# Optimization experiments

Measured on AMD Instinct MI355X. Metric: run time of the kernel, lower is better.

The kernel has to match this reference:

```python
import jax, jax.numpy as jnp
import numpy as np

H = W = 256          # input_img_height (square images)
N_NODES = 8          # camera graph nodes
N_EDGES = 64         # ~fully connected directed graph
FEAT = 1024          # edge_feat_dim
BN_EPS = 1e-5


def setup_inputs() -> dict:
    key = jax.random.key(0)
    ks = jax.random.split(key, 8)
    d = {}
    d["x"] = jax.random.normal(ks[0], (N_NODES, 3 * H * W), dtype=jnp.float32)
    d["edge_index"] = jax.random.randint(ks[1], (2, N_EDGES), 0, N_NODES)
    # ResNet stem params (conv1 replaced to take 6 channels)
    d["conv1_w"] = jax.random.normal(ks[2], (64, 6, 7, 7), dtype=jnp.float32) * 0.05
    d["bn_gamma"] = jnp.ones((64,), jnp.float32)
    d["bn_beta"] = jnp.zeros((64,), jnp.float32)
    d["bn_mean"] = jnp.zeros((64,), jnp.float32)
    d["bn_var"] = jnp.ones((64,), jnp.float32)
    d["fc_w"] = jax.random.normal(ks[3], (FEAT, 64), dtype=jnp.float32) * 0.05
    d["fc_b"] = jnp.zeros((FEAT,), jnp.float32)
    d["fc_xyz_w"] = jax.random.normal(ks[4], (3, FEAT), dtype=jnp.float32) * 0.05
    d["fc_xyz_b"] = jnp.zeros((3,), jnp.float32)
    d["fc_wpqr_w"] = jax.random.normal(ks[5], (3, FEAT), dtype=jnp.float32) * 0.05
    d["fc_wpqr_b"] = jnp.zeros((3,), jnp.float32)
    return d


def _edge_extractor(ef, conv1_w, bn_gamma, bn_beta, bn_mean, bn_var, fc_w, fc_b):
    # conv1: 6->64, 7x7, stride 2, pad 3, no bias
    y = jax.lax.conv_general_dilated(
        ef, conv1_w, window_strides=(2, 2), padding=[(3, 3), (3, 3)],
        dimension_numbers=("NCHW", "OIHW", "NCHW"))
    # BatchNorm (inference form with running stats), fused scale/shift
    scale = (bn_gamma * jax.lax.rsqrt(bn_var + BN_EPS))[None, :, None, None]
    shift = (bn_beta - bn_mean * bn_gamma * jax.lax.rsqrt(bn_var + BN_EPS))[None, :, None, None]
    y = jax.nn.relu(y * scale + shift)
    # maxpool 3x3 stride 2 pad 1
    y = jax.lax.reduce_window(y, -jnp.inf, jax.lax.max,
                              (1, 1, 3, 3), (1, 1, 2, 2),
                              [(0, 0), (0, 0), (1, 1), (1, 1)])
    # AdaptiveAvgPool2d(1) + fc to edge_feat_dim
    y = jnp.mean(y, axis=(2, 3))                     # [E, 64]
    return y @ fc_w.T + fc_b                         # [E, FEAT]


def reference(x, edge_index, conv1_w, bn_gamma, bn_beta, bn_mean, bn_var,
              fc_w, fc_b, fc_xyz_w, fc_xyz_b, fc_wpqr_w, fc_wpqr_b):
    imgs = x.reshape(N_NODES, 3, H, W)
    # compute_edge_features, vectorized: gather min/max node per edge, concat channels
    nmin = jnp.min(edge_index, axis=0)               # [E]
    nmax = jnp.max(edge_index, axis=0)               # [E]
    edge_feat = jnp.concatenate([imgs[nmin], imgs[nmax]], axis=1)  # [E, 6, H, W]
    ef = _edge_extractor(edge_feat, conv1_w, bn_gamma, bn_beta, bn_mean, bn_var, fc_w, fc_b)
    ef = jax.nn.relu(ef)
    # droprate == 0 -> no dropout
    xyz = ef @ fc_xyz_w.T + fc_xyz_b                 # [E, 3]
    wpqr = ef @ fc_wpqr_w.T + fc_wpqr_b              # [E, 3]
    full = jnp.concatenate([xyz, wpqr], axis=1)      # [E, 6]
    return (full[:N_NODES], full)
```

## Files before the change

kernel.cpp:

```cpp
#include <hip/hip_runtime.h>
#include <hip/hip_bf16.h>

#define N_NODES 8
#define N_EDGES 64
#define CO 64
#define OH 128
#define OW 128
#define FEAT 1024
#define BN_EPS 1e-5f

#define OFF_POOLED 0
#define OFF_WB     16384
#define OFF_SHIFT  65536
#define OFF_A      65792
#define OFF_B      (65792 + 16777216)

typedef short bf16x8 __attribute__((ext_vector_type(8)));
typedef float f32x4  __attribute__((ext_vector_type(4)));

__device__ __forceinline__ unsigned short f2bf(float f) {
    unsigned u = __float_as_uint(f);
    u += 0x7fffu + ((u >> 16) & 1u);
    return (unsigned short)(u >> 16);
}
__device__ __forceinline__ float blo(unsigned u) { return __uint_as_float(u << 16); }
__device__ __forceinline__ float bhi(unsigned u) { return __uint_as_float(u & 0xffff0000u); }

__global__ __launch_bounds__(256) void repack_kernel(
        const float* __restrict__ w,
        const float* __restrict__ gamma, const float* __restrict__ beta,
        const float* __restrict__ mean,  const float* __restrict__ var,
        unsigned short* __restrict__ wb2, float* __restrict__ shiftb,
        float* __restrict__ pooled) {
    int idx = blockIdx.x * 256 + threadIdx.x;
    if (idx < 2 * 64 * 192) {
        int t = idx % 192;
        int c = (idx / 192) & 63;
        int h = idx / (192 * 64);
        int rr = t >> 3, kx = t & 7;
        float val = 0.f;
        if (rr < 21 && kx < 7) {
            int ci = rr / 7, ky = rr % 7;
            float sc = gamma[c] * rsqrtf(var[c] + BN_EPS);
            val = w[((c * 6 + h * 3 + ci) * 7 + ky) * 7 + kx] * sc;
        }
        wb2[(rr * 128 + h * 64 + c) * 8 + kx] = f2bf(val);
    }
    if (idx < 64) {
        float sc = gamma[idx] * rsqrtf(var[idx] + BN_EPS);
        shiftb[idx] = beta[idx] - mean[idx] * sc;
    }
    if (idx < 64 * 64) pooled[idx] = 0.f;
}

#define RS_W 136

__global__ __launch_bounds__(512, 4) void conv_kernel(
        const float* __restrict__ x, const unsigned short* __restrict__ wb2,
        const float* __restrict__ shiftb,
        unsigned short* __restrict__ A2, unsigned short* __restrict__ B2) {
    int n  = blockIdx.x >> 7;
    int oy = blockIdx.x & 127;
    int t  = threadIdx.x;

    __shared__ __align__(16) char smem[34816];
    unsigned* rawu = (unsigned*)smem;

    const float* img = x + (size_t)n * (3 * 256 * 256);
    for (int k = t; k < 24 * RS_W; k += 512) {
        int u  = k % RS_W;
        int rr = k / RS_W;
        unsigned val = 0u;
        if (rr < 21 && u < 131) {
            int ci = (rr * 147) >> 10;
            int ky = rr - ci * 7;
            int iy = 2 * oy - 3 + ky;
            if ((unsigned)iy < 256u) {
                int c0 = 2 * u - 3;
                const float* row = img + (ci * 256 + iy) * 256;
                float f0 = ((unsigned)c0 < 256u) ? row[c0] : 0.f;
                float f1 = ((unsigned)(c0 + 1) < 256u) ? row[c0 + 1] : 0.f;
                val = (unsigned)f2bf(f0) | ((unsigned)f2bf(f1) << 16);
            }
        }
        rawu[k] = val;
    }
    __syncthreads();

    int wv = t >> 6, lane = t & 63;
    int h  = wv & 1, wg = wv >> 1;
    int quad = lane >> 4, m = lane & 15;

    f32x4 acc[4][2];
#pragma unroll
    for (int ct = 0; ct < 4; ++ct) {
        acc[ct][0] = (f32x4){0.f, 0.f, 0.f, 0.f};
        acc[ct][1] = (f32x4){0.f, 0.f, 0.f, 0.f};
    }

    const bf16x8* wbv = (const bf16x8*)wb2;

#pragma unroll 2
    for (int s = 0; s < 6; ++s) {
        int rq = 4 * s + quad;
        bf16x8 afrag[2];
#pragma unroll
        for (int nt = 0; nt < 2; ++nt) {
            int ox = 32 * wg + 16 * nt + m;
            int base = rq * RS_W + ox;
            union { unsigned u[4]; bf16x8 v; } bb;
            bb.u[0] = rawu[base];     bb.u[1] = rawu[base + 1];
            bb.u[2] = rawu[base + 2]; bb.u[3] = rawu[base + 3];
            afrag[nt] = bb.v;
        }
#pragma unroll
        for (int ct = 0; ct < 4; ++ct) {
            bf16x8 wfrag = wbv[rq * 128 + h * 64 + 16 * ct + m];
#pragma unroll
            for (int nt = 0; nt < 2; ++nt)
                acc[ct][nt] = __builtin_amdgcn_mfma_f32_16x16x32_bf16(
                                  afrag[nt], wfrag, acc[ct][nt], 0, 0, 0);
        }
    }

    float sh[4] = {0.f, 0.f, 0.f, 0.f};
    if (h) {
#pragma unroll
        for (int ct = 0; ct < 4; ++ct) sh[ct] = shiftb[16 * ct + m];
    }

    __syncthreads();
    unsigned short* T = (unsigned short*)smem;

#pragma unroll
    for (int ct = 0; ct < 4; ++ct) {
        int chp = h * 64 + 16 * ct + m;
#pragma unroll
        for (int nt = 0; nt < 2; ++nt) {
            int px0 = 32 * wg + 16 * nt + 4 * quad;
            float v0 = acc[ct][nt][0] + sh[ct];
            float v1 = acc[ct][nt][1] + sh[ct];
            float v2 = acc[ct][nt][2] + sh[ct];
            float v3 = acc[ct][nt][3] + sh[ct];
            uint2 pk;
            pk.x = (unsigned)f2bf(v0) | ((unsigned)f2bf(v1) << 16);
            pk.y = (unsigned)f2bf(v2) | ((unsigned)f2bf(v3) << 16);
            *(uint2*)&T[chp * 136 + px0] = pk;
        }
    }
    __syncthreads();

    int row = t >> 2, slot = t & 3;
    int hh = row >> 6, ch = row & 63;
    unsigned short* dst = (hh ? B2 : A2)
                        + ((size_t)(n * CO + ch) << 14) + (oy << 7) + slot * 32;
#pragma unroll
    for (int i = 0; i < 4; ++i)
        *(uint4*)(dst + i * 8) = *(uint4*)&T[row * 136 + slot * 32 + i * 8];
}

__global__ __launch_bounds__(256, 4) void pool_kernel(
        const unsigned short* __restrict__ A2,
        const unsigned short* __restrict__ B2,
        float* __restrict__ pooled) {
    int b  = blockIdx.x;
    int c  = b >> 4;
    int rt = b & 15;
    int t  = threadIdx.x;

    __shared__ unsigned short S[2 * 8 * 9 * 128];

    for (int k = t; k < 2304; k += 256) {
        int slot = k & 15;
        int r    = (k >> 4) % 9;
        int tn   = (k >> 4) / 9;
        int grow = 8 * rt - 1 + r;
        uint4 v = make_uint4(0u, 0u, 0u, 0u);
        if (grow >= 0) {
            const unsigned short* src = (tn >= 8) ? B2 : A2;
            int node = tn & 7;
            v = *(const uint4*)(src + ((size_t)(node * CO + c) << 14)
                                    + (grow << 7) + slot * 8);
        }
        *(uint4*)&S[tn * 1152 + (r << 7) + slot * 8] = v;
    }
    __syncthreads();

    int wv = t >> 6, lane = t & 63;
    int esub = lane >> 4, tc = lane & 15;

    for (int i = 0; i < 3; ++i) {
        int sidx = 12 * wv + 4 * i + esub;
        bool valid = sidx < 36;
        int ss = valid ? sidx : 0;
        int pi = 0, rem = ss;
        while (rem >= 8 - pi) { rem -= 8 - pi; ++pi; }
        int pj = pi + rem;
        const unsigned short* pa = &S[pi * 1152];
        const unsigned short* pb = &S[(8 + pj) * 1152];

        float mx[4][4];
#pragma unroll
        for (int p = 0; p < 4; ++p)
#pragma unroll
            for (int q = 0; q < 4; ++q) mx[p][q] = 0.f;

#pragma unroll
        for (int r = 0; r < 9; ++r) {
            uint4 ga = *(const uint4*)(pa + (r << 7) + tc * 8);
            uint4 gb = *(const uint4*)(pb + (r << 7) + tc * 8);
            float ha = 0.f, hb = 0.f;
            if (tc > 0) {
                ha = bhi(*(const unsigned*)(pa + (r << 7) + tc * 8 - 2));
                hb = bhi(*(const unsigned*)(pb + (r << 7) + tc * 8 - 2));
            }
            float z0 = ha + hb;
            float z1 = blo(ga.x) + blo(gb.x), z2 = bhi(ga.x) + bhi(gb.x);
            float z3 = blo(ga.y) + blo(gb.y), z4 = bhi(ga.y) + bhi(gb.y);
            float z5 = blo(ga.z) + blo(gb.z), z6 = bhi(ga.z) + bhi(gb.z);
            float z7 = blo(ga.w) + blo(gb.w), z8 = bhi(ga.w) + bhi(gb.w);
            float h0 = fmaxf(fmaxf(z0, z1), z2);
            float h1 = fmaxf(fmaxf(z2, z3), z4);
            float h2 = fmaxf(fmaxf(z4, z5), z6);
            float h3 = fmaxf(fmaxf(z6, z7), z8);
            if (r & 1) {
                int p = (r - 1) >> 1;
                mx[p][0] = fmaxf(mx[p][0], h0); mx[p][1] = fmaxf(mx[p][1], h1);
                mx[p][2] = fmaxf(mx[p][2], h2); mx[p][3] = fmaxf(mx[p][3], h3);
            } else {
                if (r >= 2) {
                    int p = (r >> 1) - 1;
                    mx[p][0] = fmaxf(mx[p][0], h0); mx[p][1] = fmaxf(mx[p][1], h1);
                    mx[p][2] = fmaxf(mx[p][2], h2); mx[p][3] = fmaxf(mx[p][3], h3);
                }
                if (r <= 6) {
                    int p = r >> 1;
                    mx[p][0] = fmaxf(mx[p][0], h0); mx[p][1] = fmaxf(mx[p][1], h1);
                    mx[p][2] = fmaxf(mx[p][2], h2); mx[p][3] = fmaxf(mx[p][3], h3);
                }
            }
        }

        float sum = 0.f;
#pragma unroll
        for (int p = 0; p < 4; ++p)
#pragma unroll
            for (int q = 0; q < 4; ++q) sum += fmaxf(mx[p][q], 0.f);

        sum += __shfl_down(sum, 8, 64);
        sum += __shfl_down(sum, 4, 64);
        sum += __shfl_down(sum, 2, 64);
        sum += __shfl_down(sum, 1, 64);
        if (tc == 0 && valid)
            atomicAdd(&pooled[((pi << 3) + pj) * 64 + c], sum);
    }
}

__global__ __launch_bounds__(256) void head_kernel(
        const int* __restrict__ ei, const float* __restrict__ pooled,
        const float* __restrict__ fc_w,   const float* __restrict__ fc_b,
        const float* __restrict__ xyz_w,  const float* __restrict__ xyz_b,
        const float* __restrict__ wpqr_w, const float* __restrict__ wpqr_b,
        float* __restrict__ out) {
    int e = blockIdx.x;
    int t = threadIdx.x;
    int a0 = ei[e], a1 = ei[N_EDGES + e];
    int code = (min(a0, a1) << 3) + max(a0, a1);
    __shared__ float pl[CO];
    if (t < CO) pl[t] = pooled[(code << 6) + t] * (1.f / 4096.f);
    __syncthreads();

    float s[6] = {0.f, 0.f, 0.f, 0.f, 0.f, 0.f};
#pragma unroll
    for (int ff = 0; ff < 4; ++ff) {
        int f = ff * 256 + t;
        const float* wr = fc_w + f * CO;
        float d = fc_b[f];
#pragma unroll
        for (int c = 0; c < CO; ++c) d = fmaf(pl[c], wr[c], d);
        d = fmaxf(d, 0.f);
#pragma unroll
        for (int r = 0; r < 3; ++r) {
            s[r]     = fmaf(d, xyz_w[r * FEAT + f],  s[r]);
            s[3 + r] = fmaf(d, wpqr_w[r * FEAT + f], s[3 + r]);
        }
    }
#pragma unroll
    for (int r = 0; r < 6; ++r)
#pragma unroll
        for (int off = 32; off > 0; off >>= 1)
            s[r] += __shfl_down(s[r], off, 64);

    __shared__ float red[4][6];
    if ((t & 63) == 0) {
#pragma unroll
        for (int r = 0; r < 6; ++r) red[t >> 6][r] = s[r];
    }
    __syncthreads();
    if (t < 6) {
        float v = red[0][t] + red[1][t] + red[2][t] + red[3][t];
        v += (t < 3) ? xyz_b[t] : wpqr_b[t - 3];
        out[48 + e * 6 + t] = v;
        if (e < 8) out[e * 6 + t] = v;
    }
}

extern "C" void kernel_launch(void* const* d_in, const int* in_sizes, int n_in,
                              void* d_out, int out_size, void* d_ws, size_t ws_size,
                              hipStream_t stream) {
    const float* x        = (const float*)d_in[0];
    const int*   ei       = (const int*)d_in[1];
    const float* conv1_w  = (const float*)d_in[2];
    const float* bn_gamma = (const float*)d_in[3];
    const float* bn_beta  = (const float*)d_in[4];
    const float* bn_mean  = (const float*)d_in[5];
    const float* bn_var   = (const float*)d_in[6];
    const float* fc_w     = (const float*)d_in[7];
    const float* fc_b     = (const float*)d_in[8];
    const float* xyz_w    = (const float*)d_in[9];
    const float* xyz_b    = (const float*)d_in[10];
    const float* wpqr_w   = (const float*)d_in[11];
    const float* wpqr_b   = (const float*)d_in[12];
    float* out = (float*)d_out;

    char* ws = (char*)d_ws;
    float*          pooled = (float*)(ws + OFF_POOLED);
    unsigned short* wb2    = (unsigned short*)(ws + OFF_WB);
    float*          shiftb = (float*)(ws + OFF_SHIFT);
    unsigned short* A2     = (unsigned short*)(ws + OFF_A);
    unsigned short* B2     = (unsigned short*)(ws + OFF_B);

    repack_kernel<<<96, 256, 0, stream>>>(conv1_w, bn_gamma, bn_beta, bn_mean,
                                          bn_var, wb2, shiftb, pooled);
    conv_kernel<<<1024, 512, 0, stream>>>(x, wb2, shiftb, A2, B2);
    pool_kernel<<<1024, 256, 0, stream>>>(A2, B2, pooled);
    head_kernel<<<64, 256, 0, stream>>>(ei, pooled, fc_w, fc_b,
                                        xyz_w, xyz_b, wpqr_w, wpqr_b, out);
}
```

Before: 137.8 us.

## Fuse four kernels into one persistent cooperative kernel with grid syncs

Replaces the repack, conv, pool and head launches with a single cooperative kernel of 256 blocks. Each block loops over four passes of conv rows and pool tiles, and grid.sync separates the stages. This is meant to remove launch overhead and the gaps between kernels. In exchange the grid is smaller, so each stage gets less parallelism and no overlap across passes, and the grid-wide barriers add their own cost.

```diff
diff --git a/kernel.cpp b/kernel.cpp
--- a/kernel.cpp
+++ b/kernel.cpp
@@ -1,5 +1,8 @@
 #include <hip/hip_runtime.h>
 #include <hip/hip_bf16.h>
+#include <hip/hip_cooperative_groups.h>
+
+namespace cg = cooperative_groups;
 
 #define N_NODES 8
 #define N_EDGES 64
@@ -15,6 +18,8 @@
 #define OFF_A      65792
 #define OFF_B      (65792 + 16777216)
 
+#define RS_W 136
+
 typedef short bf16x8 __attribute__((ext_vector_type(8)));
 typedef float f32x4  __attribute__((ext_vector_type(4)));
 
@@ -26,282 +31,294 @@
 __device__ __forceinline__ float blo(unsigned u) { return __uint_as_float(u << 16); }
 __device__ __forceinline__ float bhi(unsigned u) { return __uint_as_float(u & 0xffff0000u); }
 
-__global__ __launch_bounds__(256) void repack_kernel(
+__global__ __launch_bounds__(512, 4) void fused_kernel(
+        const float* __restrict__ x, const int* __restrict__ ei,
         const float* __restrict__ w,
         const float* __restrict__ gamma, const float* __restrict__ beta,
         const float* __restrict__ mean,  const float* __restrict__ var,
-        unsigned short* __restrict__ wb2, float* __restrict__ shiftb,
-        float* __restrict__ pooled) {
-    int idx = blockIdx.x * 256 + threadIdx.x;
-    if (idx < 2 * 64 * 192) {
-        int t = idx % 192;
-        int c = (idx / 192) & 63;
-        int h = idx / (192 * 64);
-        int rr = t >> 3, kx = t & 7;
-        float val = 0.f;
-        if (rr < 21 && kx < 7) {
-            int ci = rr / 7, ky = rr % 7;
-            float sc = gamma[c] * rsqrtf(var[c] + BN_EPS);
-            val = w[((c * 6 + h * 3 + ci) * 7 + ky) * 7 + kx] * sc;
-        }
-        wb2[(rr * 128 + h * 64 + c) * 8 + kx] = f2bf(val);
+        const float* __restrict__ fc_w,  const float* __restrict__ fc_b,
+        const float* __restrict__ xyz_w, const float* __restrict__ xyz_b,
+        const float* __restrict__ wpqr_w,const float* __restrict__ wpqr_b,
+        float* __restrict__ out,
+        float* __restrict__ pooled, unsigned short* __restrict__ wb2,
+        float* __restrict__ shiftb,
+        unsigned short* __restrict__ A2, unsigned short* __restrict__ B2) {
+    cg::grid_group grid = cg::this_grid();
+    int t   = threadIdx.x;
+    int blk = blockIdx.x;
+
+    __shared__ __align__(16) char smem[36864];
+
+    {
+        int idx = blk * 512 + t;
+        if (idx < 2 * 64 * 192) {
+            int tp = idx % 192;
+            int c  = (idx / 192) & 63;
+            int h  = idx / (192 * 64);
+            int rr = tp >> 3, kx = tp & 7;
+            float val = 0.f;
+            if (rr < 21 && kx < 7) {
+                int ci = rr / 7, ky = rr % 7;
+                float sc = gamma[c] * rsqrtf(var[c] + BN_EPS);
+                val = w[((c * 6 + h * 3 + ci) * 7 + ky) * 7 + kx] * sc;
+            }
+            wb2[(rr * 128 + h * 64 + c) * 8 + kx] = f2bf(val);
+        }
+        if (idx < 64) {
+            float sc = gamma[idx] * rsqrtf(var[idx] + BN_EPS);
+            shiftb[idx] = beta[idx] - mean[idx] * sc;
+        }
+        if (idx < 64 * 64) pooled[idx] = 0.f;
     }
-    if (idx < 64) {
-        float sc = gamma[idx] * rsqrtf(var[idx] + BN_EPS);
-        shiftb[idx] = beta[idx] - mean[idx] * sc;
+    __threadfence();
+    grid.sync();
+
+    {
+        unsigned* rawu = (unsigned*)smem;
+        int wv = t >> 6, lane = t & 63;
+        int h  = wv & 1, wg = wv >> 1;
+        int quad = lane >> 4, m = lane & 15;
+
+        for (int pass = 0; pass < 4; ++pass) {
+            int cb = pass * 256 + blk;
+            int n  = cb >> 7, oy = cb & 127;
+
+            const float* img = x + (size_t)n * (3 * 256 * 256);
+            for (int k = t; k < 24 * RS_W; k += 512) {
+                int u  = k % RS_W;
+                int rr = k / RS_W;
+                unsigned val = 0u;
+                if (rr < 21 && u < 131) {
+                    int ci = (rr * 147) >> 10;
+                    int ky = rr - ci * 7;
+                    int iy = 2 * oy - 3 + ky;
+                    if ((unsigned)iy < 256u) {
+                        int c0 = 2 * u - 3;
+                        const float* row = img + (ci * 256 + iy) * 256;
+                        float f0 = ((unsigned)c0 < 256u) ? row[c0] : 0.f;
+                        float f1 = ((unsigned)(c0 + 1) < 256u) ? row[c0 + 1] : 0.f;
+                        val = (unsigned)f2bf(f0) | ((unsigned)f2bf(f1) << 16);
+                    }
+                }
+                rawu[k] = val;
+            }
+            __syncthreads();
+
+            f32x4 acc[4][2];
+#pragma unroll
+            for (int ct = 0; ct < 4; ++ct) {
+                acc[ct][0] = (f32x4){0.f, 0.f, 0.f, 0.f};
+                acc[ct][1] = (f32x4){0.f, 0.f, 0.f, 0.f};
+            }
+
+            const bf16x8* wbv = (const bf16x8*)wb2;
+
+#pragma unroll 2
+            for (int s = 0; s < 6; ++s) {
+                int rq = 4 * s + quad;
+                bf16x8 afrag[2];
+#pragma unroll
+                for (int nt = 0; nt < 2; ++nt) {
+                    int ox = 32 * wg + 16 * nt + m;
+                    int base = rq * RS_W + ox;
+                    union { unsigned u[4]; bf16x8 v; } bb;
+                    bb.u[0] = rawu[base];     bb.u[1] = rawu[base + 1];
+                    bb.u[2] = rawu[base + 2]; bb.u[3] = rawu[base + 3];
+                    afrag[nt] = bb.v;
+                }
+#pragma unroll
+                for (int ct = 0; ct < 4; ++ct) {
+                    bf16x8 wfrag = wbv[rq * 128 + h * 64 + 16 * ct + m];
+#pragma unroll
+                    for (int nt = 0; nt < 2; ++nt)
+                        acc[ct][nt] = __builtin_amdgcn_mfma_f32_16x16x32_bf16(
+                                          afrag[nt], wfrag, acc[ct][nt], 0, 0, 0);
+                }
+            }
+
+            float sh[4] = {0.f, 0.f, 0.f, 0.f};
+            if (h) {
+#pragma unroll
+                for (int ct = 0; ct < 4; ++ct) sh[ct] = shiftb[16 * ct + m];
+            }
+
+            __syncthreads();
+            unsigned short* T = (unsigned short*)smem;
+
+#pragma unroll
+            for (int ct = 0; ct < 4; ++ct) {
+                int chp = h * 64 + 16 * ct + m;
+#pragma unroll
+                for (int nt = 0; nt < 2; ++nt) {
+                    int px0 = 32 * wg + 16 * nt + 4 * quad;
+                    float v0 = acc[ct][nt][0] + sh[ct];
+                    float v1 = acc[ct][nt][1] + sh[ct];
+                    float v2 = acc[ct][nt][2] + sh[ct];
+                    float v3 = acc[ct][nt][3] + sh[ct];
+                    uint2 pk;
+                    pk.x = (unsigned)f2bf(v0) | ((unsigned)f2bf(v1) << 16);
+                    pk.y = (unsigned)f2bf(v2) | ((unsigned)f2bf(v3) << 16);
+                    *(uint2*)&T[chp * 136 + px0] = pk;
+                }
+            }
+            __syncthreads();
+
+            int row = t >> 2, slot = t & 3;
+            int hh = row >> 6, ch = row & 63;
+            unsigned short* dst = (hh ? B2 : A2)
+                                + ((size_t)(n * CO + ch) << 14) + (oy << 7)
+                                + slot * 32;
+#pragma unroll
+            for (int i = 0; i < 4; ++i)
+                *(uint4*)(dst + i * 8) = *(uint4*)&T[row * 136 + slot * 32 + i * 8];
+            __syncthreads();
+        }
     }
-    if (idx < 64 * 64) pooled[idx] = 0.f;
-}
-
-#define RS_W 136
-
-__global__ __launch_bounds__(512, 4) void conv_kernel(
-        const float* __restrict__ x, const unsigned short* __restrict__ wb2,
-        const float* __restrict__ shiftb,
-        unsigned short* __restrict__ A2, unsigned short* __restrict__ B2) {
-    int n  = blockIdx.x >> 7;
-    int oy = blockIdx.x & 127;
-    int t  = threadIdx.x;
-
-    __shared__ __align__(16) char smem[34816];
-    unsigned* rawu = (unsigned*)smem;
-
-    const float* img = x + (size_t)n * (3 * 256 * 256);
-    for (int k = t; k < 24 * RS_W; k += 512) {
-        int u  = k % RS_W;
-        int rr = k / RS_W;
-        unsigned val = 0u;
-        if (rr < 21 && u < 131) {
-            int ci = (rr * 147) >> 10;
-            int ky = rr - ci * 7;
-            int iy = 2 * oy - 3 + ky;
-            if ((unsigned)iy < 256u) {
-                int c0 = 2 * u - 3;
-                const float* row = img + (ci * 256 + iy) * 256;
-                float f0 = ((unsigned)c0 < 256u) ? row[c0] : 0.f;
-                float f1 = ((unsigned)(c0 + 1) < 256u) ? row[c0 + 1] : 0.f;
-                val = (unsigned)f2bf(f0) | ((unsigned)f2bf(f1) << 16);
-            }
-        }
-        rawu[k] = val;
+    __threadfence();
+    grid.sync();
+
+    {
+        unsigned short* S = (unsigned short*)smem;
+        int wv = t >> 6, lane = t & 63;
+        int esub = lane >> 4, tc = lane & 15;
+
+        for (int pass = 0; pass < 4; ++pass) {
+            int pb = pass * 256 + blk;
+            int c  = pb >> 4;
+            int rt = pb & 15;
+
+            __syncthreads();
+            for (int k = t; k < 2304; k += 512) {
+                int slot = k & 15;
+                int r    = (k >> 4) % 9;
+                int tn   = (k >> 4) / 9;
+                int grow = 8 * rt - 1 + r;
+                uint4 v = make_uint4(0u, 0u, 0u, 0u);
+                if (grow >= 0) {
+                    const unsigned short* src = (tn >= 8) ? B2 : A2;
+                    int node = tn & 7;
+                    v = *(const uint4*)(src + ((size_t)(node * CO + c) << 14)
+                                            + (grow << 7) + slot * 8);
+                }
+                *(uint4*)&S[tn * 1152 + (r << 7) + slot * 8] = v;
+            }
+            __syncthreads();
+
+            for (int i = 0; i < 2; ++i) {
+                int slot0 = 32 * i + wv * 4;
+                if (slot0 >= 36) continue;
+                int sidx = slot0 + esub;
+                bool valid = sidx < 36;
+                int ss = valid ? sidx : 0;
+                int pi = 0, rem = ss;
+                while (rem >= 8 - pi) { rem -= 8 - pi; ++pi; }
+                int pj = pi + rem;
+                const unsigned short* pa  = &S[pi * 1152];
+                const unsigned short* pb2 = &S[(8 + pj) * 1152];
+
+                float mx[4][4];
+#pragma unroll
+                for (int p = 0; p < 4; ++p)
+#pragma unroll
+                    for (int q = 0; q < 4; ++q) mx[p][q] = 0.f;
+
+#pragma unroll
+                for (int r = 0; r < 9; ++r) {
+                    uint4 ga = *(const uint4*)(pa + (r << 7) + tc * 8);
+                    uint4 gb = *(const uint4*)(pb2 + (r << 7) + tc * 8);
+                    float ha = 0.f, hb = 0.f;
+                    if (tc > 0) {
+                        ha = bhi(*(const unsigned*)(pa + (r << 7) + tc * 8 - 2));
+                        hb = bhi(*(const unsigned*)(pb2 + (r << 7) + tc * 8 - 2));
+                    }
+                    float z0 = ha + hb;
+                    float z1 = blo(ga.x) + blo(gb.x), z2 = bhi(ga.x) + bhi(gb.x);
+                    float z3 = blo(ga.y) + blo(gb.y), z4 = bhi(ga.y) + bhi(gb.y);
+                    float z5 = blo(ga.z) + blo(gb.z), z6 = bhi(ga.z) + bhi(gb.z);
+                    float z7 = blo(ga.w) + blo(gb.w), z8 = bhi(ga.w) + bhi(gb.w);
+                    float h0 = fmaxf(fmaxf(z0, z1), z2);
+                    float h1 = fmaxf(fmaxf(z2, z3), z4);
+                    float h2 = fmaxf(fmaxf(z4, z5), z6);
+                    float h3 = fmaxf(fmaxf(z6, z7), z8);
+                    if (r & 1) {
+                        int p = (r - 1) >> 1;
+                        mx[p][0] = fmaxf(mx[p][0], h0); mx[p][1] = fmaxf(mx[p][1], h1);
+                        mx[p][2] = fmaxf(mx[p][2], h2); mx[p][3] = fmaxf(mx[p][3], h3);
+                    } else {
+                        if (r >= 2) {
+                            int p = (r >> 1) - 1;
+                            mx[p][0] = fmaxf(mx[p][0], h0); mx[p][1] = fmaxf(mx[p][1], h1);
+                            mx[p][2] = fmaxf(mx[p][2], h2); mx[p][3] = fmaxf(mx[p][3], h3);
+                        }
+                        if (r <= 6) {
+                            int p = r >> 1;
+                            mx[p][0] = fmaxf(mx[p][0], h0); mx[p][1] = fmaxf(mx[p][1], h1);
+                            mx[p][2] = fmaxf(mx[p][2], h2); mx[p][3] = fmaxf(mx[p][3], h3);
+                        }
+                    }
+                }
+
+                float sum = 0.f;
+#pragma unroll
+                for (int p = 0; p < 4; ++p)
+#pragma unroll
+                    for (int q = 0; q < 4; ++q) sum += fmaxf(mx[p][q], 0.f);
+
+                sum += __shfl_down(sum, 8, 64);
+                sum += __shfl_down(sum, 4, 64);
+                sum += __shfl_down(sum, 2, 64);
+                sum += __shfl_down(sum, 1, 64);
+                if (tc == 0 && valid)
+                    atomicAdd(&pooled[((pi << 3) + pj) * 64 + c], sum);
+            }
+        }
     }
-    __syncthreads();
-
-    int wv = t >> 6, lane = t & 63;
-    int h  = wv & 1, wg = wv >> 1;
-    int quad = lane >> 4, m = lane & 15;
-
-    f32x4 acc[4][2];
-#pragma unroll
-    for (int ct = 0; ct < 4; ++ct) {
-        acc[ct][0] = (f32x4){0.f, 0.f, 0.f, 0.f};
-        acc[ct][1] = (f32x4){0.f, 0.f, 0.f, 0.f};
-    }
-
-    const bf16x8* wbv = (const bf16x8*)wb2;
-
-#pragma unroll 2
-    for (int s = 0; s < 6; ++s) {
-        int rq = 4 * s + quad;
-        bf16x8 afrag[2];
-#pragma unroll
-        for (int nt = 0; nt < 2; ++nt) {
-            int ox = 32 * wg + 16 * nt + m;
-            int base = rq * RS_W + ox;
-            union { unsigned u[4]; bf16x8 v; } bb;
-            bb.u[0] = rawu[base];     bb.u[1] = rawu[base + 1];
-            bb.u[2] = rawu[base + 2]; bb.u[3] = rawu[base + 3];
-            afrag[nt] = bb.v;
-        }
-#pragma unroll
-        for (int ct = 0; ct < 4; ++ct) {
-            bf16x8 wfrag = wbv[rq * 128 + h * 64 + 16 * ct + m];
-#pragma unroll
-            for (int nt = 0; nt < 2; ++nt)
-                acc[ct][nt] = __builtin_amdgcn_mfma_f32_16x16x32_bf16(
-                                  afrag[nt], wfrag, acc[ct][nt], 0, 0, 0);
-        }
-    }
-
-    float sh[4] = {0.f, 0.f, 0.f, 0.f};
-    if (h) {
-#pragma unroll
-        for (int ct = 0; ct < 4; ++ct) sh[ct] = shiftb[16 * ct + m];
-    }
-
-    __syncthreads();
-    unsigned short* T = (unsigned short*)smem;
-
-#pragma unroll
-    for (int ct = 0; ct < 4; ++ct) {
-        int chp = h * 64 + 16 * ct + m;
-#pragma unroll
-        for (int nt = 0; nt < 2; ++nt) {
-            int px0 = 32 * wg + 16 * nt + 4 * quad;
-            float v0 = acc[ct][nt][0] + sh[ct];
-            float v1 = acc[ct][nt][1] + sh[ct];
-            float v2 = acc[ct][nt][2] + sh[ct];
-            float v3 = acc[ct][nt][3] + sh[ct];
-            uint2 pk;
-            pk.x = (unsigned)f2bf(v0) | ((unsigned)f2bf(v1) << 16);
-            pk.y = (unsigned)f2bf(v2) | ((unsigned)f2bf(v3) << 16);
-            *(uint2*)&T[chp * 136 + px0] = pk;
-        }
-    }
-    __syncthreads();
-
-    int row = t >> 2, slot = t & 3;
-    int hh = row >> 6, ch = row & 63;
-    unsigned short* dst = (hh ? B2 : A2)
-                        + ((size_t)(n * CO + ch) << 14) + (oy << 7) + slot * 32;
-#pragma unroll
-    for (int i = 0; i < 4; ++i)
-        *(uint4*)(dst + i * 8) = *(uint4*)&T[row * 136 + slot * 32 + i * 8];
-}
-
-__global__ __launch_bounds__(256, 4) void pool_kernel(
-        const unsigned short* __restrict__ A2,
-        const unsigned short* __restrict__ B2,
-        float* __restrict__ pooled) {
-    int b  = blockIdx.x;
-    int c  = b >> 4;
-    int rt = b & 15;
-    int t  = threadIdx.x;
-
-    __shared__ unsigned short S[2 * 8 * 9 * 128];
-
-    for (int k = t; k < 2304; k += 256) {
-        int slot = k & 15;
-        int r    = (k >> 4) % 9;
-        int tn   = (k >> 4) / 9;
-        int grow = 8 * rt - 1 + r;
-        uint4 v = make_uint4(0u, 0u, 0u, 0u);
-        if (grow >= 0) {
-            const unsigned short* src = (tn >= 8) ? B2 : A2;
-            int node = tn & 7;
-            v = *(const uint4*)(src + ((size_t)(node * CO + c) << 14)
-                                    + (grow << 7) + slot * 8);
-        }
-        *(uint4*)&S[tn * 1152 + (r << 7) + slot * 8] = v;
-    }
-    __syncthreads();
-
-    int wv = t >> 6, lane = t & 63;
-    int esub = lane >> 4, tc = lane & 15;
-
-    for (int i = 0; i < 3; ++i) {
-        int sidx = 12 * wv + 4 * i + esub;
-        bool valid = sidx < 36;
-        int ss = valid ? sidx : 0;
-        int pi = 0, rem = ss;
-        while (rem >= 8 - pi) { rem -= 8 - pi; ++pi; }
-        int pj = pi + rem;
-        const unsigned short* pa = &S[pi * 1152];
-        const unsigned short* pb = &S[(8 + pj) * 1152];
-
-        float mx[4][4];
-#pragma unroll
-        for (int p = 0; p < 4; ++p)
-#pragma unroll
-            for (int q = 0; q < 4; ++q) mx[p][q] = 0.f;
-
-#pragma unroll
-        for (int r = 0; r < 9; ++r) {
-            uint4 ga = *(const uint4*)(pa + (r << 7) + tc * 8);
-            uint4 gb = *(const uint4*)(pb + (r << 7) + tc * 8);
-            float ha = 0.f, hb = 0.f;
-            if (tc > 0) {
-                ha = bhi(*(const unsigned*)(pa + (r << 7) + tc * 8 - 2));
-                hb = bhi(*(const unsigned*)(pb + (r << 7) + tc * 8 - 2));
-            }
-            float z0 = ha + hb;
-            float z1 = blo(ga.x) + blo(gb.x), z2 = bhi(ga.x) + bhi(gb.x);
-            float z3 = blo(ga.y) + blo(gb.y), z4 = bhi(ga.y) + bhi(gb.y);
-            float z5 = blo(ga.z) + blo(gb.z), z6 = bhi(ga.z) + bhi(gb.z);
-            float z7 = blo(ga.w) + blo(gb.w), z8 = bhi(ga.w) + bhi(gb.w);
-            float h0 = fmaxf(fmaxf(z0, z1), z2);
-            float h1 = fmaxf(fmaxf(z2, z3), z4);
-            float h2 = fmaxf(fmaxf(z4, z5), z6);
-            float h3 = fmaxf(fmaxf(z6, z7), z8);
-            if (r & 1) {
-                int p = (r - 1) >> 1;
-                mx[p][0] = fmaxf(mx[p][0], h0); mx[p][1] = fmaxf(mx[p][1], h1);
-                mx[p][2] = fmaxf(mx[p][2], h2); mx[p][3] = fmaxf(mx[p][3], h3);
-            } else {
-                if (r >= 2) {
-                    int p = (r >> 1) - 1;
-                    mx[p][0] = fmaxf(mx[p][0], h0); mx[p][1] = fmaxf(mx[p][1], h1);
-                    mx[p][2] = fmaxf(mx[p][2], h2); mx[p][3] = fmaxf(mx[p][3], h3);
-                }
-                if (r <= 6) {
-                    int p = r >> 1;
-                    mx[p][0] = fmaxf(mx[p][0], h0); mx[p][1] = fmaxf(mx[p][1], h1);
-                    mx[p][2] = fmaxf(mx[p][2], h2); mx[p][3] = fmaxf(mx[p][3], h3);
-                }
-            }
-        }
-
-        float sum = 0.f;
-#pragma unroll
-        for (int p = 0; p < 4; ++p)
-#pragma unroll
-            for (int q = 0; q < 4; ++q) sum += fmaxf(mx[p][q], 0.f);
-
-        sum += __shfl_down(sum, 8, 64);
-        sum += __shfl_down(sum, 4, 64);
-        sum += __shfl_down(sum, 2, 64);
-        sum += __shfl_down(sum, 1, 64);
-        if (tc == 0 && valid)
-            atomicAdd(&pooled[((pi << 3) + pj) * 64 + c], sum);
-    }
-}
-
-__global__ __launch_bounds__(256) void head_kernel(
-        const int* __restrict__ ei, const float* __restrict__ pooled,
-        const float* __restrict__ fc_w,   const float* __restrict__ fc_b,
-        const float* __restrict__ xyz_w,  const float* __restrict__ xyz_b,
-        const float* __restrict__ wpqr_w, const float* __restrict__ wpqr_b,
-        float* __restrict__ out) {
-    int e = blockIdx.x;
-    int t = threadIdx.x;
-    int a0 = ei[e], a1 = ei[N_EDGES + e];
-    int code = (min(a0, a1) << 3) + max(a0, a1);
-    __shared__ float pl[CO];
-    if (t < CO) pl[t] = pooled[(code << 6) + t] * (1.f / 4096.f);
-    __syncthreads();
-
-    float s[6] = {0.f, 0.f, 0.f, 0.f, 0.f, 0.f};
-#pragma unroll
-    for (int ff = 0; ff < 4; ++ff) {
-        int f = ff * 256 + t;
-        const float* wr = fc_w + f * CO;
-        float d = fc_b[f];
-#pragma unroll
-        for (int c = 0; c < CO; ++c) d = fmaf(pl[c], wr[c], d);
-        d = fmaxf(d, 0.f);
-#pragma unroll
-        for (int r = 0; r < 3; ++r) {
-            s[r]     = fmaf(d, xyz_w[r * FEAT + f],  s[r]);
-            s[3 + r] = fmaf(d, wpqr_w[r * FEAT + f], s[3 + r]);
-        }
-    }
-#pragma unroll
-    for (int r = 0; r < 6; ++r)
-#pragma unroll
-        for (int off = 32; off > 0; off >>= 1)
-            s[r] += __shfl_down(s[r], off, 64);
-
-    __shared__ float red[4][6];
-    if ((t & 63) == 0) {
-#pragma unroll
-        for (int r = 0; r < 6; ++r) red[t >> 6][r] = s[r];
-    }
-    __syncthreads();
-    if (t < 6) {
-        float v = red[0][t] + red[1][t] + red[2][t] + red[3][t];
-        v += (t < 3) ? xyz_b[t] : wpqr_b[t - 3];
-        out[48 + e * 6 + t] = v;
-        if (e < 8) out[e * 6 + t] = v;
+    __threadfence();
+    grid.sync();
+
+    if (blk < N_EDGES) {
+        int e = blk;
+        float* pl  = (float*)smem;
+        float* red = pl + 64;
+        int a0 = ei[e], a1 = ei[N_EDGES + e];
+        int code = (min(a0, a1) << 3) + max(a0, a1);
+        if (t < CO) pl[t] = pooled[(code << 6) + t] * (1.f / 4096.f);
+        __syncthreads();
+
+        float s[6] = {0.f, 0.f, 0.f, 0.f, 0.f, 0.f};
+#pragma unroll
+        for (int ff = 0; ff < 2; ++ff) {
+            int f = ff * 512 + t;
+            const float* wr = fc_w + f * CO;
+            float d = fc_b[f];
+#pragma unroll
+            for (int c = 0; c < CO; ++c) d = fmaf(pl[c], wr[c], d);
+            d = fmaxf(d, 0.f);
+#pragma unroll
+            for (int r = 0; r < 3; ++r) {
+                s[r]     = fmaf(d, xyz_w[r * FEAT + f],  s[r]);
+                s[3 + r] = fmaf(d, wpqr_w[r * FEAT + f], s[3 + r]);
+            }
+        }
+#pragma unroll
+        for (int r = 0; r < 6; ++r)
+#pragma unroll
+            for (int off = 32; off > 0; off >>= 1)
+                s[r] += __shfl_down(s[r], off, 64);
+
+        if ((t & 63) == 0) {
+#pragma unroll
+            for (int r = 0; r < 6; ++r) red[(t >> 6) * 6 + r] = s[r];
+        }
+        __syncthreads();
+        if (t < 6) {
+            float v = 0.f;
+#pragma unroll
+            for (int wv2 = 0; wv2 < 8; ++wv2) v += red[wv2 * 6 + t];
+            v += (t < 3) ? xyz_b[t] : wpqr_b[t - 3];
+            out[48 + e * 6 + t] = v;
+            if (e < 8) out[e * 6 + t] = v;
+        }
     }
 }
 
@@ -330,10 +347,13 @@
     unsigned short* A2     = (unsigned short*)(ws + OFF_A);
     unsigned short* B2     = (unsigned short*)(ws + OFF_B);
 
-    repack_kernel<<<96, 256, 0, stream>>>(conv1_w, bn_gamma, bn_beta, bn_mean,
-                                          bn_var, wb2, shiftb, pooled);
-    conv_kernel<<<1024, 512, 0, stream>>>(x, wb2, shiftb, A2, B2);
-    pool_kernel<<<1024, 256, 0, stream>>>(A2, B2, pooled);
-    head_kernel<<<64, 256, 0, stream>>>(ei, pooled, fc_w, fc_b,
-                                        xyz_w, xyz_b, wpqr_w, wpqr_b, out);
+    void* args[] = {
+        (void*)&x, (void*)&ei, (void*)&conv1_w,
+        (void*)&bn_gamma, (void*)&bn_beta, (void*)&bn_mean, (void*)&bn_var,
+        (void*)&fc_w, (void*)&fc_b, (void*)&xyz_w, (void*)&xyz_b,
+        (void*)&wpqr_w, (void*)&wpqr_b, (void*)&out,
+        (void*)&pooled, (void*)&wb2, (void*)&shiftb, (void*)&A2, (void*)&B2
+    };
+    hipLaunchCooperativeKernel((const void*)fused_kernel, dim3(256), dim3(512),
+                               args, 0, stream);
 }
```

New measurement: 371.8 us. 170% more time.

## Fuse weight repack into conv, remap blocks per XCD, drop atomics for partial sums

Applied to the files above, without the earlier changes.

Removes the separate repack kernel: each conv block now converts and BN-scales the weights into LDS itself and computes the BN shift inline, so one launch and the global weight reads go away. The conv transpose buffer gets an XOR swizzle in place of padding to avoid LDS bank conflicts. Block indices in conv and pool are remapped so that neighbouring work lands on the same XCD for L2 locality. Pool writes per-row-tile partial sums instead of using atomicAdd, and the head kernel reduces the 16 partials. The cost is redundant weight conversion in every conv block and a larger LDS footprint that may lower occupancy.

```diff
diff --git a/kernel.cpp b/kernel.cpp
--- a/kernel.cpp
+++ b/kernel.cpp
@@ -9,11 +9,11 @@
 #define FEAT 1024
 #define BN_EPS 1e-5f
 
-#define OFF_POOLED 0
-#define OFF_WB     16384
-#define OFF_SHIFT  65536
-#define OFF_A      65792
-#define OFF_B      (65792 + 16777216)
+#define OFF_PARTIAL 0
+#define OFF_A       151552
+#define OFF_B       (151552 + 16777216)
+
+#define RS_W 136
 
 typedef short bf16x8 __attribute__((ext_vector_type(8)));
 typedef float f32x4  __attribute__((ext_vector_type(4)));
@@ -26,45 +26,39 @@
 __device__ __forceinline__ float blo(unsigned u) { return __uint_as_float(u << 16); }
 __device__ __forceinline__ float bhi(unsigned u) { return __uint_as_float(u & 0xffff0000u); }
 
-__global__ __launch_bounds__(256) void repack_kernel(
-        const float* __restrict__ w,
+__global__ __launch_bounds__(512, 4) void conv_kernel(
+        const float* __restrict__ x, const float* __restrict__ w,
         const float* __restrict__ gamma, const float* __restrict__ beta,
         const float* __restrict__ mean,  const float* __restrict__ var,
-        unsigned short* __restrict__ wb2, float* __restrict__ shiftb,
-        float* __restrict__ pooled) {
-    int idx = blockIdx.x * 256 + threadIdx.x;
-    if (idx < 2 * 64 * 192) {
-        int t = idx % 192;
-        int c = (idx / 192) & 63;
-        int h = idx / (192 * 64);
-        int rr = t >> 3, kx = t & 7;
-        float val = 0.f;
-        if (rr < 21 && kx < 7) {
-            int ci = rr / 7, ky = rr % 7;
+        unsigned short* __restrict__ A2, unsigned short* __restrict__ B2) {
+    int bx  = blockIdx.x;
+    int r16 = bx & 7;
+    int idx = bx >> 3;
+    int n   = idx >> 4;
+    int oy  = (r16 << 4) + (idx & 15);
+    int t   = threadIdx.x;
+
+    __shared__ __align__(16) char smem[62208];
+    uint4*    wl4  = (uint4*)smem;
+    unsigned* rawu = (unsigned*)(smem + 49152);
+
+    for (int k2 = t; k2 < 3072; k2 += 512) {
+        int rr  = k2 >> 7;
+        int chp = k2 & 127;
+        int h   = chp >> 6, c = chp & 63;
+        union { unsigned short s[8]; uint4 v; } pk;
+        pk.v = make_uint4(0u, 0u, 0u, 0u);
+        if (rr < 21) {
+            int ci = (rr * 147) >> 10;
+            int ky = rr - ci * 7;
             float sc = gamma[c] * rsqrtf(var[c] + BN_EPS);
-            val = w[((c * 6 + h * 3 + ci) * 7 + ky) * 7 + kx] * sc;
-        }
-        wb2[(rr * 128 + h * 64 + c) * 8 + kx] = f2bf(val);
-    }
-    if (idx < 64) {
-        float sc = gamma[idx] * rsqrtf(var[idx] + BN_EPS);
-        shiftb[idx] = beta[idx] - mean[idx] * sc;
-    }
-    if (idx < 64 * 64) pooled[idx] = 0.f;
-}
-
-#define RS_W 136
-
-__global__ __launch_bounds__(512, 4) void conv_kernel(
-        const float* __restrict__ x, const unsigned short* __restrict__ wb2,
-        const float* __restrict__ shiftb,
-        unsigned short* __restrict__ A2, unsigned short* __restrict__ B2) {
-    int n  = blockIdx.x >> 7;
-    int oy = blockIdx.x & 127;
-    int t  = threadIdx.x;
-
-    __shared__ __align__(16) char smem[34816];
-    unsigned* rawu = (unsigned*)smem;
+            const float* wr = w + ((c * 6 + h * 3 + ci) * 7 + ky) * 7;
+#pragma unroll
+            for (int kx = 0; kx < 7; ++kx)
+                pk.s[kx] = f2bf(wr[kx] * sc);
+        }
+        wl4[k2] = pk.v;
+    }
 
     const float* img = x + (size_t)n * (3 * 256 * 256);
     for (int k = t; k < 24 * RS_W; k += 512) {
@@ -98,7 +92,7 @@
         acc[ct][1] = (f32x4){0.f, 0.f, 0.f, 0.f};
     }
 
-    const bf16x8* wbv = (const bf16x8*)wb2;
+    const bf16x8* wlv = (const bf16x8*)smem;
 
 #pragma unroll 2
     for (int s = 0; s < 6; ++s) {
@@ -115,7 +109,7 @@
         }
 #pragma unroll
         for (int ct = 0; ct < 4; ++ct) {
-            bf16x8 wfrag = wbv[rq * 128 + h * 64 + 16 * ct + m];
+            bf16x8 wfrag = wlv[rq * 128 + h * 64 + 16 * ct + m];
 #pragma unroll
             for (int nt = 0; nt < 2; ++nt)
                 acc[ct][nt] = __builtin_amdgcn_mfma_f32_16x16x32_bf16(
@@ -126,7 +120,11 @@
     float sh[4] = {0.f, 0.f, 0.f, 0.f};
     if (h) {
 #pragma unroll
-        for (int ct = 0; ct < 4; ++ct) sh[ct] = shiftb[16 * ct + m];
+        for (int ct = 0; ct < 4; ++ct) {
+            int c = 16 * ct + m;
+            float sc = gamma[c] * rsqrtf(var[c] + BN_EPS);
+            sh[ct] = beta[c] - mean[c] * sc;
+        }
     }
 
     __syncthreads();
@@ -135,6 +133,7 @@
 #pragma unroll
     for (int ct = 0; ct < 4; ++ct) {
         int chp = h * 64 + 16 * ct + m;
+        int sw  = (chp & 7) << 2;
 #pragma unroll
         for (int nt = 0; nt < 2; ++nt) {
             int px0 = 32 * wg + 16 * nt + 4 * quad;
@@ -145,28 +144,35 @@
             uint2 pk;
             pk.x = (unsigned)f2bf(v0) | ((unsigned)f2bf(v1) << 16);
             pk.y = (unsigned)f2bf(v2) | ((unsigned)f2bf(v3) << 16);
-            *(uint2*)&T[chp * 136 + px0] = pk;
+            int gs = ((px0 >> 2) ^ sw);
+            *(uint2*)&T[chp * 128 + gs * 4] = pk;
         }
     }
     __syncthreads();
 
     int row = t >> 2, slot = t & 3;
     int hh = row >> 6, ch = row & 63;
+    int swr = (row & 7) << 2;
     unsigned short* dst = (hh ? B2 : A2)
                         + ((size_t)(n * CO + ch) << 14) + (oy << 7) + slot * 32;
 #pragma unroll
-    for (int i = 0; i < 4; ++i)
-        *(uint4*)(dst + i * 8) = *(uint4*)&T[row * 136 + slot * 32 + i * 8];
+    for (int i = 0; i < 4; ++i) {
+        int g  = slot * 8 + i * 2;
+        int gs = g ^ swr;
+        *(uint4*)(dst + i * 8) = *(uint4*)&T[row * 128 + gs * 4];
+    }
 }
 
 __global__ __launch_bounds__(256, 4) void pool_kernel(
         const unsigned short* __restrict__ A2,
         const unsigned short* __restrict__ B2,
-        float* __restrict__ pooled) {
-    int b  = blockIdx.x;
-    int c  = b >> 4;
-    int rt = b & 15;
-    int t  = threadIdx.x;
+        float* __restrict__ partial) {
+    int pb  = blockIdx.x;
+    int xcd = pb & 7;
+    int q   = pb >> 3;
+    int c   = q >> 1;
+    int rt  = xcd * 2 + (q & 1);
+    int t   = threadIdx.x;
 
     __shared__ unsigned short S[2 * 8 * 9 * 128];
 
@@ -196,23 +202,23 @@
         int pi = 0, rem = ss;
         while (rem >= 8 - pi) { rem -= 8 - pi; ++pi; }
         int pj = pi + rem;
-        const unsigned short* pa = &S[pi * 1152];
-        const unsigned short* pb = &S[(8 + pj) * 1152];
+        const unsigned short* pa  = &S[pi * 1152];
+        const unsigned short* pb2 = &S[(8 + pj) * 1152];
 
         float mx[4][4];
 #pragma unroll
         for (int p = 0; p < 4; ++p)
 #pragma unroll
-            for (int q = 0; q < 4; ++q) mx[p][q] = 0.f;
+            for (int qq = 0; qq < 4; ++qq) mx[p][qq] = 0.f;
 
 #pragma unroll
         for (int r = 0; r < 9; ++r) {
             uint4 ga = *(const uint4*)(pa + (r << 7) + tc * 8);
-            uint4 gb = *(const uint4*)(pb + (r << 7) + tc * 8);
+            uint4 gb = *(const uint4*)(pb2 + (r << 7) + tc * 8);
             float ha = 0.f, hb = 0.f;
             if (tc > 0) {
                 ha = bhi(*(const unsigned*)(pa + (r << 7) + tc * 8 - 2));
-                hb = bhi(*(const unsigned*)(pb + (r << 7) + tc * 8 - 2));
+                hb = bhi(*(const unsigned*)(pb2 + (r << 7) + tc * 8 - 2));
             }
             float z0 = ha + hb;
             float z1 = blo(ga.x) + blo(gb.x), z2 = bhi(ga.x) + bhi(gb.x);
@@ -245,19 +251,19 @@
 #pragma unroll
         for (int p = 0; p < 4; ++p)
 #pragma unroll
-            for (int q = 0; q < 4; ++q) sum += fmaxf(mx[p][q], 0.f);
+            for (int qq = 0; qq < 4; ++qq) sum += fmaxf(mx[p][qq], 0.f);
 
         sum += __shfl_down(sum, 8, 64);
         sum += __shfl_down(sum, 4, 64);
         sum += __shfl_down(sum, 2, 64);
         sum += __shfl_down(sum, 1, 64);
         if (tc == 0 && valid)
-            atomicAdd(&pooled[((pi << 3) + pj) * 64 + c], sum);
+            partial[(rt * 36 + sidx) * 64 + c] = sum;
     }
 }
 
 __global__ __launch_bounds__(256) void head_kernel(
-        const int* __restrict__ ei, const float* __restrict__ pooled,
+        const int* __restrict__ ei, const float* __restrict__ partial,
         const float* __restrict__ fc_w,   const float* __restrict__ fc_b,
         const float* __restrict__ xyz_w,  const float* __restrict__ xyz_b,
         const float* __restrict__ wpqr_w, const float* __restrict__ wpqr_b,
@@ -265,9 +271,16 @@
     int e = blockIdx.x;
     int t = threadIdx.x;
     int a0 = ei[e], a1 = ei[N_EDGES + e];
-    int code = (min(a0, a1) << 3) + max(a0, a1);
+    int pi = min(a0, a1), pj = max(a0, a1);
+    int rank = pi * 8 - ((pi * (pi + 1)) >> 1) + pj;
     __shared__ float pl[CO];
-    if (t < CO) pl[t] = pooled[(code << 6) + t] * (1.f / 4096.f);
+    if (t < CO) {
+        float s = 0.f;
+#pragma unroll
+        for (int rt = 0; rt < 16; ++rt)
+            s += partial[(rt * 36 + rank) * 64 + t];
+        pl[t] = s * (1.f / 4096.f);
+    }
     __syncthreads();
 
     float s[6] = {0.f, 0.f, 0.f, 0.f, 0.f, 0.f};
@@ -324,16 +337,13 @@
     float* out = (float*)d_out;
 
     char* ws = (char*)d_ws;
-    float*          pooled = (float*)(ws + OFF_POOLED);
-    unsigned short* wb2    = (unsigned short*)(ws + OFF_WB);
-    float*          shiftb = (float*)(ws + OFF_SHIFT);
-    unsigned short* A2     = (unsigned short*)(ws + OFF_A);
-    unsigned short* B2     = (unsigned short*)(ws + OFF_B);
-
-    repack_kernel<<<96, 256, 0, stream>>>(conv1_w, bn_gamma, bn_beta, bn_mean,
-                                          bn_var, wb2, shiftb, pooled);
-    conv_kernel<<<1024, 512, 0, stream>>>(x, wb2, shiftb, A2, B2);
-    pool_kernel<<<1024, 256, 0, stream>>>(A2, B2, pooled);
-    head_kernel<<<64, 256, 0, stream>>>(ei, pooled, fc_w, fc_b,
+    float*          partial = (float*)(ws + OFF_PARTIAL);
+    unsigned short* A2      = (unsigned short*)(ws + OFF_A);
+    unsigned short* B2      = (unsigned short*)(ws + OFF_B);
+
+    conv_kernel<<<1024, 512, 0, stream>>>(x, conv1_w, bn_gamma, bn_beta,
+                                          bn_mean, bn_var, A2, B2);
+    pool_kernel<<<1024, 256, 0, stream>>>(A2, B2, partial);
+    head_kernel<<<64, 256, 0, stream>>>(ei, partial, fc_w, fc_b,
                                         xyz_w, xyz_b, wpqr_w, wpqr_b, out);
 }
```

New measurement: 139.2 us. No clear change (+1.0%).
